# Performance work log

Measured on AMD Instinct MI355X. Metric: run time of the kernel, lower is better.

## Reference

```python
import jax, jax.numpy as jnp
import numpy as np

EMBED = 1024
HEADS = 16
HEAD_DIM = EMBED // HEADS
FFN = 4096
B, S = 2, 2048
EPS = 1e-5


def setup_inputs() -> dict:
    key = jax.random.key(0)
    ks = jax.random.split(key, 16)
    sc = 0.02
    return {
        "x": jax.random.normal(ks[0], (B, S, EMBED), jnp.float32),
        "rope_cos": jax.random.uniform(ks[1], (S, HEAD_DIM), jnp.float32),
        "rope_sin": jax.random.uniform(ks[2], (S, HEAD_DIM), jnp.float32),
        "Wq": jax.random.normal(ks[3], (EMBED, EMBED), jnp.float32) * sc,
        "bq": jnp.zeros((EMBED,), jnp.float32),
        "Wk": jax.random.normal(ks[4], (EMBED, EMBED), jnp.float32) * sc,
        "bk": jnp.zeros((EMBED,), jnp.float32),
        "Wv": jax.random.normal(ks[5], (EMBED, EMBED), jnp.float32) * sc,
        "bv": jnp.zeros((EMBED,), jnp.float32),
        "Wo": jax.random.normal(ks[6], (EMBED, EMBED), jnp.float32) * sc,
        "bo": jnp.zeros((EMBED,), jnp.float32),
        "W1": jax.random.normal(ks[7], (EMBED, FFN), jnp.float32) * sc,
        "b1": jnp.zeros((FFN,), jnp.float32),
        "W2": jax.random.normal(ks[8], (FFN, EMBED), jnp.float32) * sc,
        "b2": jnp.zeros((EMBED,), jnp.float32),
        "g1": jnp.ones((EMBED,), jnp.float32),
        "be1": jnp.zeros((EMBED,), jnp.float32),
        "g2": jnp.ones((EMBED,), jnp.float32),
        "be2": jnp.zeros((EMBED,), jnp.float32),
    }


def _layernorm(x, g, b):
    mu = jnp.mean(x, axis=-1, keepdims=True)
    var = jnp.var(x, axis=-1, keepdims=True)
    return (x - mu) * jax.lax.rsqrt(var + EPS) * g + b


def _rotate_half(x):
    half = x.shape[-1] // 2
    return jnp.concatenate((-x[..., half:], x[..., :half]), axis=-1)


def _apply_rope(x, cos, sin):
    # x: (B, H, S, D); cos/sin: (S, D)
    return x * cos[None, None] + _rotate_half(x) * sin[None, None]


def reference(x, rope_cos, rope_sin, Wq, bq, Wk, bk, Wv, bv, Wo, bo,
              W1, b1, W2, b2, g1, be1, g2, be2):
    batch, seq_len, embed = x.shape
    n = _layernorm(x, g1, be1)

    def heads(t):
        return t.reshape(batch, seq_len, HEADS, HEAD_DIM).transpose(0, 2, 1, 3)

    q = heads(n @ Wq + bq)
    k = heads(n @ Wk + bk)
    v = heads(n @ Wv + bv)
    q = _apply_rope(q, rope_cos, rope_sin)
    k = _apply_rope(k, rope_cos, rope_sin)

    scale = 1.0 / np.sqrt(HEAD_DIM)
    scores = jnp.einsum("bhqd,bhkd->bhqk", q, k) * scale  # (B,H,S,S)
    causal = jnp.triu(jnp.ones((seq_len, seq_len), bool), k=1)
    scores = jnp.where(causal[None, None], -jnp.inf, scores)
    attn = jax.nn.softmax(scores, axis=-1)
    out = jnp.einsum("bhqk,bhkd->bhqd", attn, v)
    out = out.transpose(0, 2, 1, 3).reshape(batch, seq_len, embed)
    x = x + (out @ Wo + bo)

    n2 = _layernorm(x, g2, be2)
    h = jax.nn.gelu(n2 @ W1 + b1, approximate=False)
    x = x + (h @ W2 + b2)
    return x
```

## Files before the change

kernel.cpp:

```cpp
#include <hip/hip_runtime.h>
#include <math.h>

#define EMBED 1024
#define SLEN  2048
#define BATCH 2
#define HEADS 16
#define HD    64
#define FFN_D 4096
#define MROWS (BATCH*SLEN)

typedef short bh8  __attribute__((ext_vector_type(8)));
typedef float f32x4 __attribute__((ext_vector_type(4)));
typedef __attribute__((address_space(3))) const short* lsp;

#define MFMA16(a,b,c) __builtin_amdgcn_mfma_f32_16x16x32_bf16((a),(b),(c),0,0,0)
#define GLDS16(g,l) __builtin_amdgcn_global_load_lds( \
    (__attribute__((address_space(1))) void*)(g), \
    (__attribute__((address_space(3))) void*)(l), 16, 0, 0)
#define DSR(dst, base, IMM) \
  asm volatile("ds_read_b128 %0, %1 offset:" #IMM : "=v"(dst) : "v"(base))

__device__ inline float b2f(short s) {
  union { unsigned u; float f; } c; c.u = ((unsigned)(unsigned short)s) << 16; return c.f;
}
__device__ inline short f2b(float f) {
  union { float f; unsigned u; } c; c.f = f;
  unsigned r = (c.u + 0x7FFFu + ((c.u >> 16) & 1u)) >> 16;
  return (short)r;
}

__global__ __launch_bounds__(256) void transpose_w(const float* __restrict__ in,
                                                   short* __restrict__ out,
                                                   int K, int N) {
  __shared__ short sm[64][65];
  const int tid = threadIdx.x;
  const int k0 = blockIdx.y * 64, n0 = blockIdx.x * 64;
#pragma unroll
  for (int it = 0; it < 16; ++it) {
    int idx = it * 256 + tid;
    int r = idx >> 6, c = idx & 63;
    sm[r][c] = f2b(in[(size_t)(k0 + r) * N + n0 + c]);
  }
  __syncthreads();
#pragma unroll
  for (int it = 0; it < 16; ++it) {
    int idx = it * 256 + tid;
    int r = idx >> 6, c = idx & 63;
    out[(size_t)(n0 + r) * K + k0 + c] = sm[c][r];
  }
}

__global__ __launch_bounds__(256) void transpose_v(const short* __restrict__ in,
                                                   short* __restrict__ out) {
  __shared__ short sm[64][65];
  const int tid = threadIdx.x;
  const int s0 = blockIdx.x * 64, bh = blockIdx.y;
  const int b = bh >> 4, h = bh & 15;
#pragma unroll
  for (int it = 0; it < 16; ++it) {
    int idx = it * 256 + tid;
    int r = idx >> 6, c = idx & 63;
    sm[r][c] = in[((size_t)(b*SLEN + s0 + r))*EMBED + h*HD + c];
  }
  __syncthreads();
#pragma unroll
  for (int it = 0; it < 16; ++it) {
    int idx = it * 256 + tid;
    int r = idx >> 6, c = idx & 63;
    out[((size_t)(bh*HD + r))*SLEN + s0 + c] = sm[c][r];
  }
}

__global__ __launch_bounds__(256) void ln_kernel(const float* __restrict__ inF,
                                                 const short* __restrict__ inB,
                                                 const float* __restrict__ gw,
                                                 const float* __restrict__ bw,
                                                 short* __restrict__ out) {
  const int row = blockIdx.x, tid = threadIdx.x;
  const int w = tid >> 6;
  const size_t base = (size_t)row * EMBED;
  float x[4];
#pragma unroll
  for (int i = 0; i < 4; ++i) {
    int c = tid + i * 256;
    x[i] = inF ? inF[base + c] : b2f(inB[base + c]);
  }
  float s = x[0] + x[1] + x[2] + x[3];
  float ss = x[0]*x[0] + x[1]*x[1] + x[2]*x[2] + x[3]*x[3];
#pragma unroll
  for (int off = 32; off >= 1; off >>= 1) { s += __shfl_xor(s, off); ss += __shfl_xor(ss, off); }
  __shared__ float red[8];
  if ((tid & 63) == 0) { red[w*2] = s; red[w*2+1] = ss; }
  __syncthreads();
  s  = red[0] + red[2] + red[4] + red[6];
  ss = red[1] + red[3] + red[5] + red[7];
  const float mu = s * (1.0f/EMBED);
  const float var = ss * (1.0f/EMBED) - mu*mu;
  const float rstd = rsqrtf(var + 1e-5f);
#pragma unroll
  for (int i = 0; i < 4; ++i) {
    int c = tid + i * 256;
    out[base + c] = f2b((x[i]-mu)*rstd*gw[c] + bw[c]);
  }
}

__global__ __launch_bounds__(256) void rope_kernel(short* __restrict__ Qb, short* __restrict__ Kb,
                                                   const float* __restrict__ cosb,
                                                   const float* __restrict__ sinb) {
  const int idx = blockIdx.x * 256 + threadIdx.x;
  const int d = idx & 31;
  const int h = (idx >> 5) & 15;
  const int s = (idx >> 9) & 2047;
  const int b = idx >> 20;
  const size_t base = ((size_t)(b*SLEN + s))*EMBED + h*HD;
  const float c0 = cosb[s*HD + d],      s0 = sinb[s*HD + d];
  const float c1 = cosb[s*HD + 32 + d], s1 = sinb[s*HD + 32 + d];
  float q0 = b2f(Qb[base + d]), q1 = b2f(Qb[base + 32 + d]);
  Qb[base + d]      = f2b(q0*c0 - q1*s0);
  Qb[base + 32 + d] = f2b(q1*c1 + q0*s1);
  float k0 = b2f(Kb[base + d]), k1 = b2f(Kb[base + 32 + d]);
  Kb[base + d]      = f2b(k0*c0 - k1*s0);
  Kb[base + 32 + d] = f2b(k1*c1 + k0*s1);
}

__global__ __launch_bounds__(256, 2) void gemm_bt(const short* __restrict__ A,
                                                  const short* __restrict__ Bt,
                                                  const float* __restrict__ bias0,
                                                  const float* __restrict__ bias1,
                                                  const float* __restrict__ bias2,
                                                  float* __restrict__ outF,
                                                  short* __restrict__ outB0,
                                                  short* __restrict__ outB1,
                                                  short* __restrict__ outB2,
                                                  const float* __restrict__ residF,
                                                  const short* __restrict__ residB,
                                                  int N, int K, int gelu, int qkv) {
  __shared__ short As[16384];
  __shared__ short Bs[16384];
  const int tid = threadIdx.x;
  const int w = tid >> 6, L = tid & 63;
  const int quad = L >> 4, l16 = L & 15;

  int bx = blockIdx.x, by = blockIdx.y;
  {
    const int gx = gridDim.x;
    const int nwg = gx * gridDim.y;
    const int wg = by*gx + bx;
    const int swz = (wg & 7)*(nwg >> 3) + (wg >> 3);
    bx = swz % gx; by = swz / gx;
  }
  const int bm = by * 128, bn = bx * 128;
  const int wm = (w >> 1) * 64, wn = (w & 1) * 64;
  const int NT = K >> 6;

  f32x4 acc[4][4];
#pragma unroll
  for (int i = 0; i < 4; ++i)
#pragma unroll
    for (int j = 0; j < 4; ++j) acc[i][j] = (f32x4){0.f,0.f,0.f,0.f};

  const int c0i = tid, c1i = 256 + tid;
  const int r0i = c0i >> 2, s0i = (c0i & 3) ^ ((r0i >> 1) & 3);
  const int r1i = c1i >> 2, s1i = (c1i & 3) ^ ((r1i >> 1) & 3);
  const short* aG0 = A  + (size_t)(bm + r0i)*K + s0i*8;
  const short* aG1 = A  + (size_t)(bm + r1i)*K + s1i*8;
  const short* bG0 = Bt + (size_t)(bn + r0i)*K + s0i*8;
  const short* bG1 = Bt + (size_t)(bn + r1i)*K + s1i*8;

  const int ssw = (l16 >> 1) & 3;
  lsp pA0 = (lsp)(As + (wm + l16)*32 + ((quad ^ ssw) << 3));
  lsp pB0 = (lsp)(Bs + (wn + l16)*32 + ((quad ^ ssw) << 3));
  lsp pA1 = pA0 + 8192;
  lsp pB1 = pB0 + 8192;

#define STG(DST, G0, G1, BUF, KH, KOFF) do { \
    GLDS16(G0 + (KOFF) + (KH)*32, DST + (BUF)*8192 + (KH)*4096 + w*512); \
    GLDS16(G1 + (KOFF) + (KH)*32, DST + (BUF)*8192 + (KH)*4096 + 2048 + w*512); \
  } while (0)

  STG(As, aG0, aG1, 0, 0, 0);   STG(Bs, bG0, bG1, 0, 0, 0);
  STG(As, aG0, aG1, 0, 1, 0);   STG(Bs, bG0, bG1, 0, 1, 0);
  STG(As, aG0, aG1, 1, 0, 64);  STG(Bs, bG0, bG1, 1, 0, 64);
  STG(As, aG0, aG1, 1, 1, 64);  STG(Bs, bG0, bG1, 1, 1, 64);

  for (int t = 0; t < NT; ++t) {
    const int cb = t & 1;
    lsp Ab = cb ? pA1 : pA0;
    lsp Bb = cb ? pB1 : pB0;
    const bool pf = (t + 2) < NT;
    const int kofA = (t + 2) << 6;
    bh8 af[4], bf[4];

    if (t < NT-1) asm volatile("s_waitcnt vmcnt(12)" ::: "memory");
    else          asm volatile("s_waitcnt vmcnt(4)"  ::: "memory");
    __builtin_amdgcn_s_barrier();
    DSR(af[0], Ab, 0);    DSR(af[1], Ab, 1024);
    DSR(af[2], Ab, 2048); DSR(af[3], Ab, 3072);
    DSR(bf[0], Bb, 0);    DSR(bf[1], Bb, 1024);
    DSR(bf[2], Bb, 2048); DSR(bf[3], Bb, 3072);
    asm volatile("s_waitcnt lgkmcnt(0)" ::: "memory");
    __builtin_amdgcn_sched_barrier(0);
    __builtin_amdgcn_s_barrier();
    if (pf) { STG(As, aG0, aG1, cb, 0, kofA); STG(Bs, bG0, bG1, cb, 0, kofA); }
    __builtin_amdgcn_sched_barrier(0);
    __builtin_amdgcn_s_setprio(1);
#pragma unroll
    for (int mi = 0; mi < 4; ++mi)
#pragma unroll
      for (int ni = 0; ni < 4; ++ni)
        acc[mi][ni] = MFMA16(af[mi], bf[ni], acc[mi][ni]);
    __builtin_amdgcn_s_setprio(0);

    if (t < NT-2)       asm volatile("s_waitcnt vmcnt(12)" ::: "memory");
    else if (t == NT-2) asm volatile("s_waitcnt vmcnt(8)"  ::: "memory");
    else                asm volatile("s_waitcnt vmcnt(0)"  ::: "memory");
    __builtin_amdgcn_s_barrier();
    DSR(af[0], Ab, 8192);  DSR(af[1], Ab, 9216);
    DSR(af[2], Ab, 10240); DSR(af[3], Ab, 11264);
    DSR(bf[0], Bb, 8192);  DSR(bf[1], Bb, 9216);
    DSR(bf[2], Bb, 10240); DSR(bf[3], Bb, 11264);
    asm volatile("s_waitcnt lgkmcnt(0)" ::: "memory");
    __builtin_amdgcn_sched_barrier(0);
    __builtin_amdgcn_s_barrier();
    if (pf) { STG(As, aG0, aG1, cb, 1, kofA); STG(Bs, bG0, bG1, cb, 1, kofA); }
    __builtin_amdgcn_sched_barrier(0);
    __builtin_amdgcn_s_setprio(1);
#pragma unroll
    for (int mi = 0; mi < 4; ++mi)
#pragma unroll
      for (int ni = 0; ni < 4; ++ni)
        acc[mi][ni] = MFMA16(af[mi], bf[ni], acc[mi][ni]);
    __builtin_amdgcn_s_setprio(0);
  }
#undef STG

#pragma unroll
  for (int mi = 0; mi < 4; ++mi) {
#pragma unroll
    for (int ni = 0; ni < 4; ++ni) {
      const int col = bn + wn + ni*16 + l16;
      float bv; short* ob2; int colw; size_t rstride;
      if (qkv) {
        const int cc = col >> 10;
        colw = col & 1023;
        bv = (cc == 0 ? bias0 : cc == 1 ? bias1 : bias2)[colw];
        ob2 = (cc == 0 ? outB0 : cc == 1 ? outB1 : outB2);
        rstride = 1024;
      } else {
        colw = col; bv = bias0 ? bias0[col] : 0.f; ob2 = outB0; rstride = N;
      }
#pragma unroll
      for (int r = 0; r < 4; ++r) {
        const int gr = bm + wm + mi*16 + quad*4 + r;
        float v = acc[mi][ni][r] + bv;
        if (gelu) v = 0.5f*v*(1.f + erff(v*0.70710678f));
        if (residF) v += residF[(size_t)gr*N + col];
        if (residB) v += b2f(residB[(size_t)gr*N + col]);
        if (outF) outF[(size_t)gr*N + col] = v;
        if (ob2)  ob2[(size_t)gr*rstride + colw] = f2b(v);
      }
    }
  }
}

__global__ __launch_bounds__(256) void attn_kernel(const short* __restrict__ Qb,
                                                   const short* __restrict__ Kb,
                                                   const short* __restrict__ VT,
                                                   short* __restrict__ AOb) {
  __shared__ short Klds[64*72];
  __shared__ short Vlds[64*72];
  __shared__ short Plds[4*16*72];
  const int tid = threadIdx.x;
  const int w = tid >> 6, L = tid & 63, quad = L >> 4, l16 = L & 15;
  const int bh = blockIdx.x, qt = 31 - (int)blockIdx.y;
  const int b = bh >> 4, h = bh & 15;
  const int qbase = qt*64 + w*16;

  const size_t qrow = ((size_t)(b*SLEN + qbase + l16))*EMBED + h*HD;
  const bh8 aq0 = *(const bh8*)(Qb + qrow + quad*8);
  const bh8 aq1 = *(const bh8*)(Qb + qrow + 32 + quad*8);

  f32x4 o[4];
#pragma unroll
  for (int i = 0; i < 4; ++i) o[i] = (f32x4){0.f,0.f,0.f,0.f};
  float m_r[4] = {-1e30f,-1e30f,-1e30f,-1e30f};
  float l_r[4] = {0.f,0.f,0.f,0.f};
  const float scale = 0.125f;
  const size_t kg = ((size_t)(b*SLEN))*EMBED + h*HD;
  const size_t vg = ((size_t)(bh*HD))*SLEN;
  const int r0 = tid >> 3, ch = tid & 7;

  for (int kt = 0; kt <= qt; ++kt) {
    const int k0 = kt*64;
    __syncthreads();
    *(bh8*)(Klds + r0*72 + ch*8)      = *(const bh8*)(Kb + kg + (size_t)(k0 + r0)*EMBED + ch*8);
    *(bh8*)(Klds + (r0+32)*72 + ch*8) = *(const bh8*)(Kb + kg + (size_t)(k0 + r0 + 32)*EMBED + ch*8);
    *(bh8*)(Vlds + r0*72 + ch*8)      = *(const bh8*)(VT + vg + (size_t)r0*SLEN + k0 + ch*8);
    *(bh8*)(Vlds + (r0+32)*72 + ch*8) = *(const bh8*)(VT + vg + (size_t)(r0+32)*SLEN + k0 + ch*8);
    __syncthreads();

    f32x4 s[4];
#pragma unroll
    for (int nt = 0; nt < 4; ++nt) {
      s[nt] = (f32x4){0.f,0.f,0.f,0.f};
      const short* kp = Klds + (nt*16 + l16)*72 + quad*8;
      s[nt] = MFMA16(aq0, *(const bh8*)kp,        s[nt]);
      s[nt] = MFMA16(aq1, *(const bh8*)(kp + 32), s[nt]);
    }

    const bool lastTile = (kt == qt);
#pragma unroll
    for (int r = 0; r < 4; ++r) {
      const int q = qbase + quad*4 + r;
      float v[4];
#pragma unroll
      for (int nt = 0; nt < 4; ++nt) {
        v[nt] = s[nt][r]*scale;
        if (lastTile && (k0 + nt*16 + l16 > q)) v[nt] = -1e30f;
      }
      float mx = fmaxf(fmaxf(v[0], v[1]), fmaxf(v[2], v[3]));
#pragma unroll
      for (int off = 8; off >= 1; off >>= 1) mx = fmaxf(mx, __shfl_xor(mx, off));
      const float mnew = fmaxf(m_r[r], mx);
      const float alpha = __expf(m_r[r] - mnew);
      float p[4], rs = 0.f;
#pragma unroll
      for (int nt = 0; nt < 4; ++nt) { p[nt] = __expf(v[nt] - mnew); rs += p[nt]; }
#pragma unroll
      for (int off = 8; off >= 1; off >>= 1) rs += __shfl_xor(rs, off);
      l_r[r] = l_r[r]*alpha + rs;
      m_r[r] = mnew;
#pragma unroll
      for (int dt = 0; dt < 4; ++dt) o[dt][r] *= alpha;
      short* prow = Plds + w*1152 + (quad*4 + r)*72;
#pragma unroll
      for (int nt = 0; nt < 4; ++nt) prow[nt*16 + l16] = f2b(p[nt]);
    }

    const short* pr = Plds + w*1152 + l16*72;
    const bh8 pf0 = *(const bh8*)(pr + quad*8);
    const bh8 pf1 = *(const bh8*)(pr + 32 + quad*8);
#pragma unroll
    for (int dt = 0; dt < 4; ++dt) {
      const short* vp = Vlds + (dt*16 + l16)*72 + quad*8;
      o[dt] = MFMA16(pf0, *(const bh8*)vp,        o[dt]);
      o[dt] = MFMA16(pf1, *(const bh8*)(vp + 32), o[dt]);
    }
  }

#pragma unroll
  for (int r = 0; r < 4; ++r) {
    const float inv = 1.0f / l_r[r];
    const size_t orow = ((size_t)(b*SLEN + qbase + quad*4 + r))*EMBED + h*HD;
#pragma unroll
    for (int dt = 0; dt < 4; ++dt)
      AOb[orow + dt*16 + l16] = f2b(o[dt][r]*inv);
  }
}

extern "C" void kernel_launch(void* const* d_in, const int* in_sizes, int n_in,
                              void* d_out, int out_size, void* d_ws, size_t ws_size,
                              hipStream_t stream) {
  const float* x    = (const float*)d_in[0];
  const float* cosb = (const float*)d_in[1];
  const float* sinb = (const float*)d_in[2];
  const float* Wq = (const float*)d_in[3];  const float* bq  = (const float*)d_in[4];
  const float* Wk = (const float*)d_in[5];  const float* bk  = (const float*)d_in[6];
  const float* Wv = (const float*)d_in[7];  const float* bv  = (const float*)d_in[8];
  const float* Wo = (const float*)d_in[9];  const float* bo  = (const float*)d_in[10];
  const float* W1 = (const float*)d_in[11]; const float* b1  = (const float*)d_in[12];
  const float* W2 = (const float*)d_in[13]; const float* b2  = (const float*)d_in[14];
  const float* g1 = (const float*)d_in[15]; const float* be1 = (const float*)d_in[16];
  const float* g2 = (const float*)d_in[17]; const float* be2 = (const float*)d_in[18];
  float* out = (float*)d_out;

  char* ws = (char*)d_ws;
  const size_t MB = 1ull << 20;
  short* wqkvT = (short*)(ws + 0*MB);
  short* woT = (short*)(ws + 6*MB);
  short* w1T = (short*)(ws + 8*MB);
  short* n1b = (short*)(ws + 16*MB);
  short* Qb  = (short*)(ws + 24*MB);
  short* Kb  = (short*)(ws + 32*MB);
  short* Vb  = (short*)(ws + 40*MB);
  short* VTb = (short*)(ws + 48*MB);
  short* AOb = (short*)(ws + 56*MB);
  float* X1f = (float*)(ws + 16*MB);
  short* n2b = (short*)(ws + 0*MB);
  short* Hb  = (short*)(ws + 32*MB);
  short* w2T = (short*)(ws + 0*MB);

  transpose_w<<<dim3(16,16), 256, 0, stream>>>(Wq, wqkvT,                1024, 1024);
  transpose_w<<<dim3(16,16), 256, 0, stream>>>(Wk, wqkvT + 1024*1024,    1024, 1024);
  transpose_w<<<dim3(16,16), 256, 0, stream>>>(Wv, wqkvT + 2*1024*1024,  1024, 1024);
  transpose_w<<<dim3(16,16), 256, 0, stream>>>(Wo, woT, 1024, 1024);
  transpose_w<<<dim3(64,16), 256, 0, stream>>>(W1, w1T, 1024, 4096);

  ln_kernel<<<MROWS, 256, 0, stream>>>(x, nullptr, g1, be1, n1b);

  gemm_bt<<<dim3(24,32), 256, 0, stream>>>(n1b, wqkvT, bq, bk, bv,
                                           nullptr, Qb, Kb, Vb, nullptr, nullptr,
                                           3072, 1024, 0, 1);

  rope_kernel<<<8192, 256, 0, stream>>>(Qb, Kb, cosb, sinb);

  transpose_v<<<dim3(32,32), 256, 0, stream>>>(Vb, VTb);

  attn_kernel<<<dim3(32,32), 256, 0, stream>>>(Qb, Kb, VTb, AOb);

  gemm_bt<<<dim3(8,32), 256, 0, stream>>>(AOb, woT, bo, nullptr, nullptr,
                                          X1f, nullptr, nullptr, nullptr, x, nullptr,
                                          1024, 1024, 0, 0);

  ln_kernel<<<MROWS, 256, 0, stream>>>(X1f, nullptr, g2, be2, n2b);

  gemm_bt<<<dim3(32,32), 256, 0, stream>>>(n2b, w1T, b1, nullptr, nullptr,
                                           nullptr, Hb, nullptr, nullptr, nullptr, nullptr,
                                           4096, 1024, 1, 0);

  transpose_w<<<dim3(16,64), 256, 0, stream>>>(W2, w2T, 4096, 1024);

  gemm_bt<<<dim3(8,32), 256, 0, stream>>>(Hb, w2T, b2, nullptr, nullptr,
                                          out, nullptr, nullptr, nullptr, X1f, nullptr,
                                          1024, 4096, 0, 0);
}
```

Measured before the change: 455.4 us.

## Fuse RoPE into QKV GEMM epilogue, double-buffer attention K/V, use exp2

Drops the standalone RoPE kernel and applies the rotation inside the QKV GEMM epilogue, where each wave's 64-column slice holds one full head, so Q and K are no longer re-read and re-written. The attention kernel now double-buffers its K/V tiles in LDS and prefetches the next tile into registers while computing the current one, which removes one barrier per iteration. Softmax folds log2(e) into the scale and uses the hardware v_exp_f32 (exp2) instruction. The costs are more LDS per attention block and extra cos/sin loads in the GEMM epilogue.

Measured after the change: 425.4 us. 1.07x faster.

```diff
diff --git a/kernel.cpp b/kernel.cpp
--- a/kernel.cpp
+++ b/kernel.cpp
@@ -27,6 +27,9 @@
   union { float f; unsigned u; } c; c.f = f;
   unsigned r = (c.u + 0x7FFFu + ((c.u >> 16) & 1u)) >> 16;
   return (short)r;
+}
+__device__ inline float exp2a(float x) {
+  float r; asm("v_exp_f32 %0, %1" : "=v"(r) : "v"(x)); return r;
 }
 
 __global__ __launch_bounds__(256) void transpose_w(const float* __restrict__ in,
@@ -102,25 +105,6 @@
     int c = tid + i * 256;
     out[base + c] = f2b((x[i]-mu)*rstd*gw[c] + bw[c]);
   }
-}
-
-__global__ __launch_bounds__(256) void rope_kernel(short* __restrict__ Qb, short* __restrict__ Kb,
-                                                   const float* __restrict__ cosb,
-                                                   const float* __restrict__ sinb) {
-  const int idx = blockIdx.x * 256 + threadIdx.x;
-  const int d = idx & 31;
-  const int h = (idx >> 5) & 15;
-  const int s = (idx >> 9) & 2047;
-  const int b = idx >> 20;
-  const size_t base = ((size_t)(b*SLEN + s))*EMBED + h*HD;
-  const float c0 = cosb[s*HD + d],      s0 = sinb[s*HD + d];
-  const float c1 = cosb[s*HD + 32 + d], s1 = sinb[s*HD + 32 + d];
-  float q0 = b2f(Qb[base + d]), q1 = b2f(Qb[base + 32 + d]);
-  Qb[base + d]      = f2b(q0*c0 - q1*s0);
-  Qb[base + 32 + d] = f2b(q1*c1 + q0*s1);
-  float k0 = b2f(Kb[base + d]), k1 = b2f(Kb[base + 32 + d]);
-  Kb[base + d]      = f2b(k0*c0 - k1*s0);
-  Kb[base + 32 + d] = f2b(k1*c1 + k0*s1);
 }
 
 __global__ __launch_bounds__(256, 2) void gemm_bt(const short* __restrict__ A,
@@ -134,6 +118,8 @@
                                                   short* __restrict__ outB2,
                                                   const float* __restrict__ residF,
                                                   const short* __restrict__ residB,
+                                                  const float* __restrict__ ropeCos,
+                                                  const float* __restrict__ ropeSin,
                                                   int N, int K, int gelu, int qkv) {
   __shared__ short As[16384];
   __shared__ short Bs[16384];
@@ -234,21 +220,52 @@
   }
 #undef STG
 
+  if (qkv) {
+    const int cc = (bn + wn) >> 10;
+    const float* bp = (cc == 0 ? bias0 : cc == 1 ? bias1 : bias2);
+    short* ob2 = (cc == 0 ? outB0 : cc == 1 ? outB1 : outB2);
+#pragma unroll
+    for (int mi = 0; mi < 4; ++mi) {
+      float vv[4][4];
+#pragma unroll
+      for (int ni = 0; ni < 4; ++ni) {
+        const int colw = (bn + wn + ni*16 + l16) & 1023;
+#pragma unroll
+        for (int r = 0; r < 4; ++r) vv[ni][r] = acc[mi][ni][r] + bp[colw];
+      }
+      if (cc <= 1) {
+#pragma unroll
+        for (int nlo = 0; nlo < 2; ++nlo) {
+          const int d = nlo*16 + l16;
+#pragma unroll
+          for (int r = 0; r < 4; ++r) {
+            const int s = (bm + wm + mi*16 + quad*4 + r) & (SLEN - 1);
+            const float c0 = ropeCos[s*HD + d],      s0 = ropeSin[s*HD + d];
+            const float c1 = ropeCos[s*HD + 32 + d], s1 = ropeSin[s*HD + 32 + d];
+            const float lo = vv[nlo][r], hi = vv[nlo + 2][r];
+            vv[nlo][r]     = lo*c0 - hi*s0;
+            vv[nlo + 2][r] = hi*c1 + lo*s1;
+          }
+        }
+      }
+#pragma unroll
+      for (int ni = 0; ni < 4; ++ni) {
+        const int colw = (bn + wn + ni*16 + l16) & 1023;
+#pragma unroll
+        for (int r = 0; r < 4; ++r) {
+          const int gr = bm + wm + mi*16 + quad*4 + r;
+          ob2[(size_t)gr*1024 + colw] = f2b(vv[ni][r]);
+        }
+      }
+    }
+    return;
+  }
 #pragma unroll
   for (int mi = 0; mi < 4; ++mi) {
 #pragma unroll
     for (int ni = 0; ni < 4; ++ni) {
       const int col = bn + wn + ni*16 + l16;
-      float bv; short* ob2; int colw; size_t rstride;
-      if (qkv) {
-        const int cc = col >> 10;
-        colw = col & 1023;
-        bv = (cc == 0 ? bias0 : cc == 1 ? bias1 : bias2)[colw];
-        ob2 = (cc == 0 ? outB0 : cc == 1 ? outB1 : outB2);
-        rstride = 1024;
-      } else {
-        colw = col; bv = bias0 ? bias0[col] : 0.f; ob2 = outB0; rstride = N;
-      }
+      const float bv = bias0 ? bias0[col] : 0.f;
 #pragma unroll
       for (int r = 0; r < 4; ++r) {
         const int gr = bm + wm + mi*16 + quad*4 + r;
@@ -257,7 +274,7 @@
         if (residF) v += residF[(size_t)gr*N + col];
         if (residB) v += b2f(residB[(size_t)gr*N + col]);
         if (outF) outF[(size_t)gr*N + col] = v;
-        if (ob2)  ob2[(size_t)gr*rstride + colw] = f2b(v);
+        if (outB0) outB0[(size_t)gr*N + col] = f2b(v);
       }
     }
   }
@@ -267,8 +284,8 @@
                                                    const short* __restrict__ Kb,
                                                    const short* __restrict__ VT,
                                                    short* __restrict__ AOb) {
-  __shared__ short Klds[64*72];
-  __shared__ short Vlds[64*72];
+  __shared__ short Klds[2][64*72];
+  __shared__ short Vlds[2][64*72];
   __shared__ short Plds[4*16*72];
   const int tid = threadIdx.x;
   const int w = tid >> 6, L = tid & 63, quad = L >> 4, l16 = L & 15;
@@ -285,25 +302,40 @@
   for (int i = 0; i < 4; ++i) o[i] = (f32x4){0.f,0.f,0.f,0.f};
   float m_r[4] = {-1e30f,-1e30f,-1e30f,-1e30f};
   float l_r[4] = {0.f,0.f,0.f,0.f};
-  const float scale = 0.125f;
-  const size_t kg = ((size_t)(b*SLEN))*EMBED + h*HD;
-  const size_t vg = ((size_t)(bh*HD))*SLEN;
+  const float scale2 = 0.125f * 1.44269504089f;
+  const short* KgP = Kb + ((size_t)(b*SLEN))*EMBED + h*HD;
+  const short* VgP = VT + ((size_t)(bh*HD))*SLEN;
   const int r0 = tid >> 3, ch = tid & 7;
 
+  bh8 k0r, k1r, v0r, v1r;
+  k0r = *(const bh8*)(KgP + (size_t)r0*EMBED + ch*8);
+  k1r = *(const bh8*)(KgP + (size_t)(r0 + 32)*EMBED + ch*8);
+  v0r = *(const bh8*)(VgP + (size_t)r0*SLEN + ch*8);
+  v1r = *(const bh8*)(VgP + (size_t)(r0 + 32)*SLEN + ch*8);
+
+  int cur = 0;
   for (int kt = 0; kt <= qt; ++kt) {
+    short* Kl = Klds[cur];
+    short* Vl = Vlds[cur];
+    *(bh8*)(Kl + r0*72 + ch*8)      = k0r;
+    *(bh8*)(Kl + (r0+32)*72 + ch*8) = k1r;
+    *(bh8*)(Vl + r0*72 + ch*8)      = v0r;
+    *(bh8*)(Vl + (r0+32)*72 + ch*8) = v1r;
+    __syncthreads();
+    if (kt < qt) {
+      const int kk = (kt + 1)*64;
+      k0r = *(const bh8*)(KgP + (size_t)(kk + r0)*EMBED + ch*8);
+      k1r = *(const bh8*)(KgP + (size_t)(kk + r0 + 32)*EMBED + ch*8);
+      v0r = *(const bh8*)(VgP + (size_t)r0*SLEN + kk + ch*8);
+      v1r = *(const bh8*)(VgP + (size_t)(r0 + 32)*SLEN + kk + ch*8);
+    }
+
     const int k0 = kt*64;
-    __syncthreads();
-    *(bh8*)(Klds + r0*72 + ch*8)      = *(const bh8*)(Kb + kg + (size_t)(k0 + r0)*EMBED + ch*8);
-    *(bh8*)(Klds + (r0+32)*72 + ch*8) = *(const bh8*)(Kb + kg + (size_t)(k0 + r0 + 32)*EMBED + ch*8);
-    *(bh8*)(Vlds + r0*72 + ch*8)      = *(const bh8*)(VT + vg + (size_t)r0*SLEN + k0 + ch*8);
-    *(bh8*)(Vlds + (r0+32)*72 + ch*8) = *(const bh8*)(VT + vg + (size_t)(r0+32)*SLEN + k0 + ch*8);
-    __syncthreads();
-
     f32x4 s[4];
 #pragma unroll
     for (int nt = 0; nt < 4; ++nt) {
       s[nt] = (f32x4){0.f,0.f,0.f,0.f};
-      const short* kp = Klds + (nt*16 + l16)*72 + quad*8;
+      const short* kp = Kl + (nt*16 + l16)*72 + quad*8;
       s[nt] = MFMA16(aq0, *(const bh8*)kp,        s[nt]);
       s[nt] = MFMA16(aq1, *(const bh8*)(kp + 32), s[nt]);
     }
@@ -315,17 +347,17 @@
       float v[4];
 #pragma unroll
       for (int nt = 0; nt < 4; ++nt) {
-        v[nt] = s[nt][r]*scale;
+        v[nt] = s[nt][r]*scale2;
         if (lastTile && (k0 + nt*16 + l16 > q)) v[nt] = -1e30f;
       }
       float mx = fmaxf(fmaxf(v[0], v[1]), fmaxf(v[2], v[3]));
 #pragma unroll
       for (int off = 8; off >= 1; off >>= 1) mx = fmaxf(mx, __shfl_xor(mx, off));
       const float mnew = fmaxf(m_r[r], mx);
-      const float alpha = __expf(m_r[r] - mnew);
+      const float alpha = exp2a(m_r[r] - mnew);
       float p[4], rs = 0.f;
 #pragma unroll
-      for (int nt = 0; nt < 4; ++nt) { p[nt] = __expf(v[nt] - mnew); rs += p[nt]; }
+      for (int nt = 0; nt < 4; ++nt) { p[nt] = exp2a(v[nt] - mnew); rs += p[nt]; }
 #pragma unroll
       for (int off = 8; off >= 1; off >>= 1) rs += __shfl_xor(rs, off);
       l_r[r] = l_r[r]*alpha + rs;
@@ -342,10 +374,11 @@
     const bh8 pf1 = *(const bh8*)(pr + 32 + quad*8);
 #pragma unroll
     for (int dt = 0; dt < 4; ++dt) {
-      const short* vp = Vlds + (dt*16 + l16)*72 + quad*8;
+      const short* vp = Vl + (dt*16 + l16)*72 + quad*8;
       o[dt] = MFMA16(pf0, *(const bh8*)vp,        o[dt]);
       o[dt] = MFMA16(pf1, *(const bh8*)(vp + 32), o[dt]);
     }
+    cur ^= 1;
   }
 
 #pragma unroll
@@ -400,9 +433,7 @@
 
   gemm_bt<<<dim3(24,32), 256, 0, stream>>>(n1b, wqkvT, bq, bk, bv,
                                            nullptr, Qb, Kb, Vb, nullptr, nullptr,
-                                           3072, 1024, 0, 1);
-
-  rope_kernel<<<8192, 256, 0, stream>>>(Qb, Kb, cosb, sinb);
+                                           cosb, sinb, 3072, 1024, 0, 1);
 
   transpose_v<<<dim3(32,32), 256, 0, stream>>>(Vb, VTb);
 
@@ -410,17 +441,17 @@
 
   gemm_bt<<<dim3(8,32), 256, 0, stream>>>(AOb, woT, bo, nullptr, nullptr,
                                           X1f, nullptr, nullptr, nullptr, x, nullptr,
-                                          1024, 1024, 0, 0);
+                                          nullptr, nullptr, 1024, 1024, 0, 0);
 
   ln_kernel<<<MROWS, 256, 0, stream>>>(X1f, nullptr, g2, be2, n2b);
 
   gemm_bt<<<dim3(32,32), 256, 0, stream>>>(n2b, w1T, b1, nullptr, nullptr,
                                            nullptr, Hb, nullptr, nullptr, nullptr, nullptr,
-                                           4096, 1024, 1, 0);
+                                           nullptr, nullptr, 4096, 1024, 1, 0);
 
   transpose_w<<<dim3(16,64), 256, 0, stream>>>(W2, w2T, 4096, 1024);
 
   gemm_bt<<<dim3(8,32), 256, 0, stream>>>(Hb, w2T, b2, nullptr, nullptr,
                                           out, nullptr, nullptr, nullptr, X1f, nullptr,
-                                          1024, 4096, 0, 0);
-}
+                                          nullptr, nullptr, 1024, 4096, 0, 0);
+}
```
